# Optimization experiments

Measured on AMD Instinct MI355X. Metric: run time of the kernel, lower is better.

## Reference

```python
import jax, jax.numpy as jnp
import numpy as np

K = 3  # torch_geometric knn_interpolate default
EPS = 1e-16


def knn_interpolate(l_y, l_pos, h_pos):
    # squared distances [N_h, N_l]
    d2 = jnp.sum((h_pos[:, None, :] - l_pos[None, :, :]) ** 2, axis=-1)
    neg_d, idx = jax.lax.top_k(-d2, K)          # k nearest: idx [N_h, K]
    w = 1.0 / jnp.maximum(-neg_d, EPS)           # inverse squared-distance weights
    feats = l_y[idx]                             # [N_h, K, F] gather
    return jnp.sum(w[..., None] * feats, axis=1) / jnp.sum(w, axis=1, keepdims=True)


def mlp(x, W1, b1, W2, b2, W3, b3):
    x = jax.nn.relu(x @ W1 + b1)
    x = jax.nn.relu(x @ W2 + b2)
    return x @ W3 + b3


def setup_inputs() -> dict:
    key = jax.random.key(0)
    ks = jax.random.split(key, 8)
    N_h, N_l, H, O = 32768, 8192, 512, 128
    s1 = 1.0 / np.sqrt(H)
    return {
        "emb": jax.random.normal(ks[0], (N_h, H), jnp.float32),
        "l_y": jax.random.normal(ks[1], (N_l, O), jnp.float32),
        "l_pos": jax.random.uniform(ks[2], (N_l, 3), jnp.float32),
        "h_pos": jax.random.uniform(ks[3], (N_h, 3), jnp.float32),
        "W1": jax.random.normal(ks[4], (H, H), jnp.float32) * s1,
        "b1": jnp.zeros((H,), jnp.float32),
        "W2": jax.random.normal(ks[5], (H, H), jnp.float32) * s1,
        "b2": jnp.zeros((H,), jnp.float32),
        "W3": jax.random.normal(ks[6], (H, O), jnp.float32) * s1,
        "b3": jnp.zeros((O,), jnp.float32),
    }


def reference(emb, l_y, l_pos, h_pos, W1, b1, W2, b2, W3, b3):
    x = mlp(emb, W1, b1, W2, b2, W3, b3)
    return x + knn_interpolate(l_y, l_pos, h_pos)
```

## Files before the change

kernel.cpp:

```cpp
#include <hip/hip_runtime.h>
#include <stdint.h>

typedef __attribute__((ext_vector_type(4))) float f32x4;
typedef __attribute__((ext_vector_type(8))) short bf16x8;
typedef __attribute__((ext_vector_type(4))) unsigned short u16x4;

#define AS1(p) ((const __attribute__((address_space(1))) void*)(p))
#define AS3(p) ((__attribute__((address_space(3))) void*)(p))

__device__ __forceinline__ unsigned short f2bf(float f){
  unsigned u = __builtin_bit_cast(unsigned, f);
  u += 0x7FFF + ((u >> 16) & 1);
  return (unsigned short)(u >> 16);
}

template<int N> __device__ __forceinline__ void waitcnt_vm(){
  if constexpr (N==0) asm volatile("s_waitcnt vmcnt(0)" ::: "memory");
  else if constexpr (N==2) asm volatile("s_waitcnt vmcnt(2)" ::: "memory");
  else if constexpr (N==4) asm volatile("s_waitcnt vmcnt(4)" ::: "memory");
  else if constexpr (N==5) asm volatile("s_waitcnt vmcnt(5)" ::: "memory");
  else if constexpr (N==6) asm volatile("s_waitcnt vmcnt(6)" ::: "memory");
}

__global__ __launch_bounds__(256) void k_transpose3(const float* __restrict__ W1,
                                                    const float* __restrict__ W2,
                                                    const float* __restrict__ W3,
                                                    unsigned short* __restrict__ W1t,
                                                    unsigned short* __restrict__ W2t,
                                                    unsigned short* __restrict__ W3t){
  const int z = blockIdx.z;
  const float* in; unsigned short* out; int R, C;
  if (z == 0){ in = W1; out = W1t; R = 512; C = 512; }
  else if (z == 1){ in = W2; out = W2t; R = 512; C = 512; }
  else { in = W3; out = W3t; R = 512; C = 128; if (blockIdx.x >= 4) return; }
  __shared__ float tile[32][33];
  int tx = threadIdx.x & 31, ty = threadIdx.x >> 5;
  int c0 = blockIdx.x*32, r0 = blockIdx.y*32;
  #pragma unroll
  for (int i = 0; i < 4; i++)
    tile[ty + i*8][tx] = in[(size_t)(r0 + ty + i*8)*C + c0 + tx];
  __syncthreads();
  #pragma unroll
  for (int i = 0; i < 4; i++)
    out[(size_t)(c0 + ty + i*8)*R + r0 + tx] = f2bf(tile[tx][ty + i*8]);
}

template<int NC, int TW, bool AF32, bool RELU, bool OUTBF16, bool ADDOUT>
__global__ __launch_bounds__(TW, 2) void k_gemm(const void* __restrict__ Av,
                                                const unsigned short* __restrict__ Bt,
                                                const float* __restrict__ bias,
                                                void* __restrict__ out, int K){
  constexpr int WARPS_N = TW/128;
  constexpr int WN = NC/WARPS_N;
  constexpr int NI = WN/16;
  constexpr int IA = AF32 ? 0 : (128*4)/TW;
  constexpr int IB = (NC*4)/TW;
  constexpr int LS = IA + IB;

  __shared__ short As[3][128*32];
  __shared__ short Bs[3][NC*32];

  const int tid  = threadIdx.x;
  const int lane = tid & 63, wid = tid >> 6;
  const int wr = wid / WARPS_N, wc = wid % WARPS_N;
  const int l15 = lane & 15, lk = lane >> 4;
  const int bm = blockIdx.x;

  const unsigned short* Bsrc[IB];
  #pragma unroll
  for (int q = 0; q < IB; q++){
    int row = q*(TW/4) + (tid >> 2);
    int ch  = (tid & 3) ^ ((row >> 1) & 3);
    Bsrc[q] = Bt + (size_t)row*K + ch*8;
  }
  const unsigned short* Asrc16[IA > 0 ? IA : 1];
  if constexpr (!AF32){
    #pragma unroll
    for (int a = 0; a < IA; a++){
      int row = a*(TW/4) + (tid >> 2);
      int ch  = (tid & 3) ^ ((row >> 1) & 3);
      Asrc16[a] = (const unsigned short*)Av + (size_t)bm*128*K + (size_t)row*K + ch*8;
    }
  }
  const float* A32 = (const float*)Av + (size_t)bm*128*K + (size_t)(tid>>2)*K + (size_t)(tid&3)*8;
  const int woff = (tid >> 2)*32 + ((tid & 3) ^ (((tid >> 2) >> 1) & 3))*8;

#define STAGE_B(t_, bb_) do{ int k0_ = (t_) << 5; _Pragma("unroll") \
  for (int q = 0; q < IB; q++) \
    __builtin_amdgcn_global_load_lds(AS1(Bsrc[q] + k0_), AS3(&Bs[bb_][(q*(TW/4))*32 + tid*8]), 16, 0, 0); \
}while(0)
#define STAGE_A16(t_, bb_) do{ int k0_ = (t_) << 5; _Pragma("unroll") \
  for (int a = 0; a < IA; a++) \
    __builtin_amdgcn_global_load_lds(AS1(Asrc16[a] + k0_), AS3(&As[bb_][(a*(TW/4))*32 + tid*8]), 16, 0, 0); \
}while(0)
#define A_CONV_WRITE(bb_) do{ bf16x8 p_; _Pragma("unroll") \
  for (int j_ = 0; j_ < 4; j_++){ p_[j_] = (short)f2bf(ra0[j_]); p_[j_+4] = (short)f2bf(ra1[j_]); } \
  *(bf16x8*)&As[bb_][woff] = p_; \
}while(0)

  f32x4 acc[4][NI];
  #pragma unroll
  for (int i = 0; i < 4; i++)
    #pragma unroll
    for (int j = 0; j < NI; j++) acc[i][j] = (f32x4){0.f,0.f,0.f,0.f};

  const int nt = K >> 5;
  f32x4 ra0, ra1;

  if constexpr (AF32){
    ra0 = *(const f32x4*)(A32);
    ra1 = *(const f32x4*)(A32 + 4);
    STAGE_B(0, 0);
    STAGE_B(1, 1);
    waitcnt_vm<4>();
    A_CONV_WRITE(0);
    asm volatile("s_waitcnt lgkmcnt(0)" ::: "memory");
  } else {
    STAGE_A16(0, 0); STAGE_B(0, 0);
    STAGE_A16(1, 1); STAGE_B(1, 1);
    waitcnt_vm<LS>();
  }
  __builtin_amdgcn_s_barrier();

  int b = 0;
  for (int t = 0; t < nt; ++t){
    bf16x8 af[4], bg[NI];
    #pragma unroll
    for (int i = 0; i < 4; i++){
      int R = wr*64 + i*16 + l15;
      af[i] = *(const bf16x8*)&As[b][R*32 + (lk ^ ((R >> 1) & 3))*8];
    }
    #pragma unroll
    for (int j = 0; j < NI; j++){
      int R = wc*WN + j*16 + l15;
      bg[j] = *(const bf16x8*)&Bs[b][R*32 + (lk ^ ((R >> 1) & 3))*8];
    }

    int b2 = b + 2; if (b2 >= 3) b2 -= 3;
    if constexpr (AF32){
      if (t + 1 < nt){
        int k1 = (t + 1) << 5;
        ra0 = *(const f32x4*)(A32 + k1);
        ra1 = *(const f32x4*)(A32 + k1 + 4);
      }
      if (t + 2 < nt) STAGE_B(t + 2, b2);
    } else {
      if (t + 2 < nt){ STAGE_A16(t + 2, b2); STAGE_B(t + 2, b2); }
    }

    __builtin_amdgcn_s_setprio(1);
    #pragma unroll
    for (int i = 0; i < 4; i++)
      #pragma unroll
      for (int j = 0; j < NI; j++)
        acc[i][j] = __builtin_amdgcn_mfma_f32_16x16x32_bf16(af[i], bg[j], acc[i][j], 0, 0, 0);
    __builtin_amdgcn_s_setprio(0);

    if (t + 2 < nt) waitcnt_vm<(AF32 ? 4 : LS)>();
    else            waitcnt_vm<0>();
    if constexpr (AF32){
      if (t + 1 < nt){
        int wb = b + 1; if (wb >= 3) wb -= 3;
        A_CONV_WRITE(wb);
      }
    }
    asm volatile("s_waitcnt lgkmcnt(0)" ::: "memory");
    __builtin_amdgcn_s_barrier();
    b = (b + 1 == 3) ? 0 : b + 1;
  }
#undef STAGE_B
#undef STAGE_A16
#undef A_CONV_WRITE

  const int row0 = bm*128 + wr*64 + lk*4;
  const int col0 = wc*WN + l15;
  #pragma unroll
  for (int i = 0; i < 4; i++){
    #pragma unroll
    for (int j = 0; j < NI; j++){
      int col = col0 + j*16;
      float bv = bias[col];
      #pragma unroll
      for (int r = 0; r < 4; r++){
        int row = row0 + i*16 + r;
        float v = acc[i][j][r] + bv;
        if (RELU) v = fmaxf(v, 0.f);
        if (ADDOUT) v = v + ((const float*)out)[(size_t)row*NC + col];
        if (OUTBF16) ((unsigned short*)out)[(size_t)row*NC + col] = f2bf(v);
        else         ((float*)out)[(size_t)row*NC + col] = v;
      }
    }
  }
}

#define GD 14
#define GD3 (GD*GD*GD)
#define NL 8192

__device__ __forceinline__ int cellcoord(float x){
  int c = (int)(x * (float)GD);
  return min(GD-1, max(0, c));
}

__global__ __launch_bounds__(64) void k_zero(int* __restrict__ p){
  #pragma unroll
  for (int i = 0; i < 16; i++)
    ((int4*)p)[threadIdx.x*16 + i] = (int4){0,0,0,0};
}

__global__ __launch_bounds__(256) void k_hist(const float* __restrict__ l_pos,
                                              int* __restrict__ hist){
  int i = blockIdx.x*256 + threadIdx.x;
  float x = l_pos[3*i], y = l_pos[3*i+1], z = l_pos[3*i+2];
  int c = (cellcoord(z)*GD + cellcoord(y))*GD + cellcoord(x);
  atomicAdd(&hist[c], 1);
}

__global__ __launch_bounds__(1024) void k_scan(const int* __restrict__ hist,
                                               int* __restrict__ cellStart,
                                               int* __restrict__ cursor){
  __shared__ int s[1024];
  int t = threadIdx.x;
  int4 v = ((const int4*)hist)[t];
  int sum = v.x + v.y + v.z + v.w;
  s[t] = sum;
  __syncthreads();
  for (int off = 1; off < 1024; off <<= 1){
    int val = (t >= off) ? s[t-off] : 0;
    __syncthreads();
    s[t] += val;
    __syncthreads();
  }
  int base = s[t] - sum;
  int4 cs;
  cs.x = base;
  cs.y = base + v.x;
  cs.z = base + v.x + v.y;
  cs.w = base + v.x + v.y + v.z;
  ((int4*)cellStart)[t] = cs;
  ((int4*)cursor)[t]    = cs;
}

__global__ __launch_bounds__(256) void k_scatter(const float* __restrict__ l_pos,
                                                 int* __restrict__ cursor,
                                                 float4* __restrict__ sorted){
  int i = blockIdx.x*256 + threadIdx.x;
  float x = l_pos[3*i], y = l_pos[3*i+1], z = l_pos[3*i+2];
  int c = (cellcoord(z)*GD + cellcoord(y))*GD + cellcoord(x);
  int slot = atomicAdd(&cursor[c], 1);
  float4 q; q.x = x; q.y = y; q.z = z; q.w = __int_as_float(i);
  sorted[slot] = q;
}

#define KNN_INS(dv, gi) \
  if (gi != i0 && gi != i1 && gi != i2 && \
      (dv < d2 || (dv == d2 && gi < i2))){ \
    if (dv < d1 || (dv == d1 && gi < i1)){ \
      d2 = d1; i2 = i1; \
      if (dv < d0 || (dv == d0 && gi < i0)){ d1 = d0; i1 = i0; d0 = dv; i0 = gi; } \
      else { d1 = dv; i1 = gi; } \
    } else { d2 = dv; i2 = gi; } \
  }

#define KNN_MERGE16() \
  _Pragma("unroll") \
  for (int m = 1; m < 16; m <<= 1){ \
    float e0 = __shfl_xor(d0, m), e1 = __shfl_xor(d1, m), e2 = __shfl_xor(d2, m); \
    int   j0 = __shfl_xor(i0, m), j1 = __shfl_xor(i1, m), j2 = __shfl_xor(i2, m); \
    KNN_INS(e0, j0); KNN_INS(e1, j1); KNN_INS(e2, j2); \
  }

__global__ __launch_bounds__(256) void k_knn_grid(const float* __restrict__ h_pos,
                                                  const int* __restrict__ cellStart,
                                                  const float4* __restrict__ sorted,
                                                  float* __restrict__ w,
                                                  int* __restrict__ idx){
  const int t = blockIdx.x*256 + threadIdx.x;
  const int h = t >> 4, sl = t & 15;
  const float hx = h_pos[3*h], hy = h_pos[3*h+1], hz = h_pos[3*h+2];
  const int cx = cellcoord(hx), cy = cellcoord(hy), cz = cellcoord(hz);
  const float cs = 1.0f/(float)GD;
  float d0 = 3e38f, d1 = 3e38f, d2 = 3e38f;
  int   i0 = 0x7fffffff, i1 = 0x7fffffff, i2 = 0x7fffffff;

  for (int ci = sl; ci < 27; ci += 16){
    int dz = ci/9 - 1, dy = (ci - (ci/9)*9)/3 - 1, dx = ci % 3 - 1;
    int zz = cz+dz, yy = cy+dy, xx = cx+dx;
    if ((unsigned)zz >= GD || (unsigned)yy >= GD || (unsigned)xx >= GD) continue;
    int c = (zz*GD + yy)*GD + xx;
    int p0 = cellStart[c], p1 = cellStart[c+1];
    for (int p = p0; p < p1; p++){
      float4 qq = sorted[p];
      float ddx = hx - qq.x, ddy = hy - qq.y, ddz = hz - qq.z;
      float d = fmaf(ddx, ddx, fmaf(ddy, ddy, ddz*ddz));
      int gi = __float_as_int(qq.w);
      KNN_INS(d, gi);
    }
  }
  KNN_MERGE16();

  for (int r = 2; r < GD; r++){
    int rp = r - 1;
    float B = 3e38f;
    if (cx - rp > 0)      B = fminf(B, hx - (float)(cx-rp)*cs);
    if (cx + rp + 1 < GD) B = fminf(B, (float)(cx+rp+1)*cs - hx);
    if (cy - rp > 0)      B = fminf(B, hy - (float)(cy-rp)*cs);
    if (cy + rp + 1 < GD) B = fminf(B, (float)(cy+rp+1)*cs - hy);
    if (cz - rp > 0)      B = fminf(B, hz - (float)(cz-rp)*cs);
    if (cz + rp + 1 < GD) B = fminf(B, (float)(cz+rp+1)*cs - hz);
    if (d2 <= B*B) break;

    int side = 2*r + 1, ss = side*side, tot = ss*side;
    for (int ci = sl; ci < tot; ci += 16){
      int dz = ci/ss - r;
      int rem = ci - (ci/ss)*ss;
      int dy = rem/side - r, dx = rem - (rem/side)*side - r;
      int adx = abs(dx), ady = abs(dy), adz = abs(dz);
      if (max(adx, max(ady, adz)) < r) continue;
      int zz = cz+dz, yy = cy+dy, xx = cx+dx;
      if ((unsigned)zz >= GD || (unsigned)yy >= GD || (unsigned)xx >= GD) continue;
      int c = (zz*GD + yy)*GD + xx;
      int p0 = cellStart[c], p1 = cellStart[c+1];
      for (int p = p0; p < p1; p++){
        float4 qq = sorted[p];
        float ddx = hx - qq.x, ddy = hy - qq.y, ddz = hz - qq.z;
        float d = fmaf(ddx, ddx, fmaf(ddy, ddy, ddz*ddz));
        int gi = __float_as_int(qq.w);
        KNN_INS(d, gi);
      }
    }
    KNN_MERGE16();
  }

  if (sl == 0){
    w[3*h+0] = 1.0f/fmaxf(d0, 1e-16f); idx[3*h+0] = i0;
    w[3*h+1] = 1.0f/fmaxf(d1, 1e-16f); idx[3*h+1] = i1;
    w[3*h+2] = 1.0f/fmaxf(d2, 1e-16f); idx[3*h+2] = i2;
  }
}

__global__ __launch_bounds__(256) void k_knn_gather(const float* __restrict__ w,
                                                    const int* __restrict__ idx,
                                                    const float* __restrict__ l_y,
                                                    float* __restrict__ out){
  const int t = blockIdx.x*256 + threadIdx.x;
  const int h = t >> 5, lane = t & 31;
  const float w0 = w[h*3+0], w1 = w[h*3+1], w2 = w[h*3+2];
  const int   j0 = idx[h*3+0], j1 = idx[h*3+1], j2 = idx[h*3+2];
  const f32x4* ly4 = (const f32x4*)l_y;
  f32x4 a = ly4[(size_t)j0*32 + lane]*w0
          + ly4[(size_t)j1*32 + lane]*w1
          + ly4[(size_t)j2*32 + lane]*w2;
  float inv = 1.0f/(w0 + w1 + w2);
  ((f32x4*)out)[(size_t)h*32 + lane] = a*inv;
}

extern "C" void kernel_launch(void* const* d_in, const int* in_sizes, int n_in,
                              void* d_out, int out_size, void* d_ws, size_t ws_size,
                              hipStream_t stream){
  const float* emb   = (const float*)d_in[0];
  const float* l_y   = (const float*)d_in[1];
  const float* l_pos = (const float*)d_in[2];
  const float* h_pos = (const float*)d_in[3];
  const float* W1    = (const float*)d_in[4];
  const float* b1    = (const float*)d_in[5];
  const float* W2    = (const float*)d_in[6];
  const float* b2    = (const float*)d_in[7];
  const float* W3    = (const float*)d_in[8];
  const float* b3    = (const float*)d_in[9];

  const int M = 32768, H = 512;

  char* ws = (char*)d_ws;
  unsigned short* bufA = (unsigned short*)(ws);
  unsigned short* bufB = (unsigned short*)(ws + 33554432);
  unsigned short* W1t  = (unsigned short*)(ws + 67108864);
  unsigned short* W2t  = (unsigned short*)(ws + 67633152);
  unsigned short* W3t  = (unsigned short*)(ws + 68157440);
  int*    hist      = (int*)   (ws + 68288512);
  int*    cellStart = (int*)   (ws + 68304896);
  int*    cursor    = (int*)   (ws + 68321280);
  float4* sorted    = (float4*)(ws + 68354048);
  float* wts = (float*)(ws + 74579968);
  int*   idx = (int*)  (ws + 74973184);

  k_transpose3<<<dim3(16, 16, 3), 256, 0, stream>>>(W1, W2, W3, W1t, W2t, W3t);

  k_zero<<<dim3(1), 64, 0, stream>>>(hist);
  k_hist<<<dim3(NL/256), 256, 0, stream>>>(l_pos, hist);
  k_scan<<<dim3(1), 1024, 0, stream>>>(hist, cellStart, cursor);
  k_scatter<<<dim3(NL/256), 256, 0, stream>>>(l_pos, cursor, sorted);
  k_knn_grid<<<dim3(M*16/256), 256, 0, stream>>>(h_pos, cellStart, sorted, wts, idx);
  k_knn_gather<<<dim3(M*32/256), 256, 0, stream>>>(wts, idx, l_y, (float*)d_out);

  k_gemm<512, 512, true,  true,  true,  false><<<dim3(M/128), 512, 0, stream>>>(emb,  W1t, b1, bufB, H);
  k_gemm<512, 512, false, true,  true,  false><<<dim3(M/128), 512, 0, stream>>>(bufB, W2t, b2, bufA, H);
  k_gemm<128, 256, false, false, false, true ><<<dim3(M/128), 256, 0, stream>>>(bufA, W3t, b3, d_out, H);
}
```

Baseline: 122.9 us.

## Split GEMM N dimension across blocks and shrink third-GEMM M tile

Generalizes the GEMM kernel with BM and a 2D grid so the two 512-wide layers run as 128x256 tiles over two column blocks, with a higher minimum-occupancy bound. The final 128-wide GEMM uses 64-row tiles, doubling its block count. The goal is more resident blocks and better CU fill on a device with many CUs. In exchange each A tile is loaded twice for layers 1 and 2, and the fp32 embedding is re-read and re-converted per column block.

Measured after the change: 120.0 us. 1.02x faster.

```diff
diff --git a/kernel.cpp b/kernel.cpp
--- a/kernel.cpp
+++ b/kernel.cpp
@@ -17,8 +17,8 @@
 template<int N> __device__ __forceinline__ void waitcnt_vm(){
   if constexpr (N==0) asm volatile("s_waitcnt vmcnt(0)" ::: "memory");
   else if constexpr (N==2) asm volatile("s_waitcnt vmcnt(2)" ::: "memory");
+  else if constexpr (N==3) asm volatile("s_waitcnt vmcnt(3)" ::: "memory");
   else if constexpr (N==4) asm volatile("s_waitcnt vmcnt(4)" ::: "memory");
-  else if constexpr (N==5) asm volatile("s_waitcnt vmcnt(5)" ::: "memory");
   else if constexpr (N==6) asm volatile("s_waitcnt vmcnt(6)" ::: "memory");
 }
 
@@ -45,33 +45,34 @@
     out[(size_t)(c0 + ty + i*8)*R + r0 + tx] = f2bf(tile[tx][ty + i*8]);
 }
 
-template<int NC, int TW, bool AF32, bool RELU, bool OUTBF16, bool ADDOUT>
-__global__ __launch_bounds__(TW, 2) void k_gemm(const void* __restrict__ Av,
-                                                const unsigned short* __restrict__ Bt,
-                                                const float* __restrict__ bias,
-                                                void* __restrict__ out, int K){
-  constexpr int WARPS_N = TW/128;
+template<int BM, int NC, int TW, int MINW, bool AF32, bool RELU, bool OUTBF16, bool ADDOUT>
+__global__ __launch_bounds__(TW, MINW) void k_gemm(const void* __restrict__ Av,
+                                                   const unsigned short* __restrict__ Bt,
+                                                   const float* __restrict__ bias,
+                                                   void* __restrict__ out, int K){
+  constexpr int WARPS_M = BM/64;
+  constexpr int WARPS_N = (TW/64)/WARPS_M;
   constexpr int WN = NC/WARPS_N;
   constexpr int NI = WN/16;
-  constexpr int IA = AF32 ? 0 : (128*4)/TW;
+  constexpr int IA = AF32 ? 0 : (BM*4)/TW;
   constexpr int IB = (NC*4)/TW;
   constexpr int LS = IA + IB;
 
-  __shared__ short As[3][128*32];
+  __shared__ short As[3][BM*32];
   __shared__ short Bs[3][NC*32];
 
   const int tid  = threadIdx.x;
   const int lane = tid & 63, wid = tid >> 6;
   const int wr = wid / WARPS_N, wc = wid % WARPS_N;
   const int l15 = lane & 15, lk = lane >> 4;
-  const int bm = blockIdx.x;
+  const int bm = blockIdx.x, bn = blockIdx.y;
 
   const unsigned short* Bsrc[IB];
   #pragma unroll
   for (int q = 0; q < IB; q++){
     int row = q*(TW/4) + (tid >> 2);
     int ch  = (tid & 3) ^ ((row >> 1) & 3);
-    Bsrc[q] = Bt + (size_t)row*K + ch*8;
+    Bsrc[q] = Bt + (size_t)bn*NC*K + (size_t)row*K + ch*8;
   }
   const unsigned short* Asrc16[IA > 0 ? IA : 1];
   if constexpr (!AF32){
@@ -79,10 +80,10 @@
     for (int a = 0; a < IA; a++){
       int row = a*(TW/4) + (tid >> 2);
       int ch  = (tid & 3) ^ ((row >> 1) & 3);
-      Asrc16[a] = (const unsigned short*)Av + (size_t)bm*128*K + (size_t)row*K + ch*8;
-    }
-  }
-  const float* A32 = (const float*)Av + (size_t)bm*128*K + (size_t)(tid>>2)*K + (size_t)(tid&3)*8;
+      Asrc16[a] = (const unsigned short*)Av + (size_t)bm*BM*K + (size_t)row*K + ch*8;
+    }
+  }
+  const float* A32 = (const float*)Av + (size_t)bm*BM*K + (size_t)(tid>>2)*K + (size_t)(tid&3)*8;
   const int woff = (tid >> 2)*32 + ((tid & 3) ^ (((tid >> 2) >> 1) & 3))*8;
 
 #define STAGE_B(t_, bb_) do{ int k0_ = (t_) << 5; _Pragma("unroll") \
@@ -112,7 +113,7 @@
     ra1 = *(const f32x4*)(A32 + 4);
     STAGE_B(0, 0);
     STAGE_B(1, 1);
-    waitcnt_vm<4>();
+    waitcnt_vm<IB>();
     A_CONV_WRITE(0);
     asm volatile("s_waitcnt lgkmcnt(0)" ::: "memory");
   } else {
@@ -156,7 +157,7 @@
         acc[i][j] = __builtin_amdgcn_mfma_f32_16x16x32_bf16(af[i], bg[j], acc[i][j], 0, 0, 0);
     __builtin_amdgcn_s_setprio(0);
 
-    if (t + 2 < nt) waitcnt_vm<(AF32 ? 4 : LS)>();
+    if (t + 2 < nt) waitcnt_vm<(AF32 ? IB : LS)>();
     else            waitcnt_vm<0>();
     if constexpr (AF32){
       if (t + 1 < nt){
@@ -172,8 +173,9 @@
 #undef STAGE_A16
 #undef A_CONV_WRITE
 
-  const int row0 = bm*128 + wr*64 + lk*4;
-  const int col0 = wc*WN + l15;
+  const int row0 = bm*BM + wr*64 + lk*4;
+  const int col0 = bn*NC + wc*WN + l15;
+  const int NOUT = NC*gridDim.y;
   #pragma unroll
   for (int i = 0; i < 4; i++){
     #pragma unroll
@@ -185,9 +187,9 @@
         int row = row0 + i*16 + r;
         float v = acc[i][j][r] + bv;
         if (RELU) v = fmaxf(v, 0.f);
-        if (ADDOUT) v = v + ((const float*)out)[(size_t)row*NC + col];
-        if (OUTBF16) ((unsigned short*)out)[(size_t)row*NC + col] = f2bf(v);
-        else         ((float*)out)[(size_t)row*NC + col] = v;
+        if (ADDOUT) v = v + ((const float*)out)[(size_t)row*NOUT + col];
+        if (OUTBF16) ((unsigned short*)out)[(size_t)row*NOUT + col] = f2bf(v);
+        else         ((float*)out)[(size_t)row*NOUT + col] = v;
       }
     }
   }
@@ -393,7 +395,7 @@
   k_knn_grid<<<dim3(M*16/256), 256, 0, stream>>>(h_pos, cellStart, sorted, wts, idx);
   k_knn_gather<<<dim3(M*32/256), 256, 0, stream>>>(wts, idx, l_y, (float*)d_out);
 
-  k_gemm<512, 512, true,  true,  true,  false><<<dim3(M/128), 512, 0, stream>>>(emb,  W1t, b1, bufB, H);
-  k_gemm<512, 512, false, true,  true,  false><<<dim3(M/128), 512, 0, stream>>>(bufB, W2t, b2, bufA, H);
-  k_gemm<128, 256, false, false, false, true ><<<dim3(M/128), 256, 0, stream>>>(bufA, W3t, b3, d_out, H);
-}
+  k_gemm<128, 256, 512, 4, true,  true,  true,  false><<<dim3(M/128, 2), 512, 0, stream>>>(emb,  W1t, b1, bufB, H);
+  k_gemm<128, 256, 512, 4, false, true,  true,  false><<<dim3(M/128, 2), 512, 0, stream>>>(bufB, W2t, b2, bufA, H);
+  k_gemm<64,  128, 256, 2, false, false, false, true ><<<dim3(M/64,  1), 256, 0, stream>>>(bufA, W3t, b3, d_out, H);
+}
```
